# Optimization experiments

Measured on AMD Instinct MI355X. Metric: run time of the kernel, lower is better.

The kernel has to match this reference:

```python
import jax, jax.numpy as jnp
import numpy as np

B, TK, H = 32, 1024, 512
N = 2 * H          # hidden_dim * 2
AD = 512           # attention_dimension


def setup_inputs() -> dict:
    key = jax.random.key(0)
    ks = jax.random.split(key, 11)
    s = 0.02  # weight scale
    return {
        's_t_hat': jax.random.normal(ks[0], (B, N), jnp.float32),
        'encoder_outputs': jax.random.normal(ks[1], (B, TK, N), jnp.float32),
        'encoder_feature': jax.random.normal(ks[2], (B * TK, N), jnp.float32),
        'enc_padding_mask': jax.random.uniform(ks[3], (B, TK), jnp.float32),
        'coverage': jax.random.uniform(ks[4], (B, TK), jnp.float32),
        'r_i': jax.random.normal(ks[5], (B, TK, AD), jnp.float32),
        'W_s_w': jax.random.normal(ks[6], (N, N), jnp.float32) * s,
        'W_s_b': jax.random.normal(ks[7], (N,), jnp.float32) * s,
        'W_c_w': jax.random.normal(ks[8], (N, 1), jnp.float32) * s,
        'v_w': jax.random.normal(ks[9], (1, N), jnp.float32) * s,
        'W_r_w': jax.random.normal(ks[10], (N, AD), jnp.float32) * s,
    }


def reference(s_t_hat, encoder_outputs, encoder_feature, enc_padding_mask,
              coverage, r_i, W_s_w, W_s_b, W_c_w, v_w, W_r_w):
    b, t_k, n = encoder_outputs.shape
    # decoder feature: W_s(s_t_hat), broadcast over time
    dec_fea = s_t_hat @ W_s_w.T + W_s_b                       # [b, n]
    enc_feat = encoder_feature.reshape(b, t_k, n)             # [b, t_k, n]
    # coverage feature: W_c applied to scalar coverage per position
    cov_feat = coverage[..., None] * W_c_w[:, 0]              # [b, t_k, n]
    e = jnp.tanh(enc_feat + dec_fea[:, None, :] + cov_feat)   # [b, t_k, n]
    scores = jnp.einsum('btn,n->bt', e, v_w[0])               # [b, t_k]
    attn_ = jax.nn.softmax(scores, axis=1) * enc_padding_mask
    attn = attn_ / attn_.sum(1, keepdims=True)                # renormalized
    c_t = jnp.einsum('bt,btn->bn', attn, encoder_outputs)     # [b, n]
    coverage_new = coverage + attn                            # [b, t_k]
    # structural (LSA) branch
    Wrri = jnp.einsum('bta,na->btn', r_i, W_r_w)              # [b, t_k, n]
    e_s = jnp.tanh(Wrri + dec_fea[:, None, :])
    s2 = jnp.einsum('btn,n->bt', e_s, v_w[0])
    a_struct = (jax.nn.softmax(s2, axis=1) * enc_padding_mask)[:, None, :]  # [b,1,t_k]
    c_t_struct = jnp.einsum('bt,btn->bn', a_struct[:, 0], encoder_outputs)  # [b, n]
    return (c_t, attn, coverage_new, c_t_struct, a_struct)
```

## Files before the change

kernel.cpp:

```cpp
#include <hip/hip_runtime.h>
#include <hip/hip_bf16.h>

static constexpr int BB   = 32;
static constexpr int TKK  = 1024;
static constexpr int ND   = 1024;
static constexpr int ADIM = 512;

typedef __attribute__((ext_vector_type(8))) short bf16x8;
typedef __attribute__((ext_vector_type(4))) float f32x4;

__device__ __forceinline__ float fast_tanh(float x) {
  x = fminf(fmaxf(x, -15.f), 15.f);
  float e = __expf(2.f * x);
  return __fdividef(e - 1.f, e + 1.f);
}

__device__ __forceinline__ short f2bf(float x) {
  unsigned u = __float_as_uint(x);
  u += 0x7FFF + ((u >> 16) & 1);
  return (short)(u >> 16);
}

__device__ __forceinline__ void gload_lds16(const void* g, void* l) {
  __builtin_amdgcn_global_load_lds(
      (const __attribute__((address_space(1))) unsigned int*)g,
      (__attribute__((address_space(3))) unsigned int*)l, 16, 0, 0);
}

__global__ __launch_bounds__(256) void k_cvt2(const float* __restrict__ r_i,
    const float* __restrict__ Wr, short* __restrict__ rb, short* __restrict__ wb) {
  size_t bid = blockIdx.x;
  const float* src;
  short* dst;
  size_t i;
  if (bid < 8192) { src = r_i; dst = rb; i = bid * 256 + threadIdx.x; }
  else            { src = Wr;  dst = wb; i = (bid - 8192) * 256 + threadIdx.x; }
  float4 a = ((const float4*)src)[2 * i];
  float4 b = ((const float4*)src)[2 * i + 1];
  bf16x8 h;
  h[0] = f2bf(a.x); h[1] = f2bf(a.y); h[2] = f2bf(a.z); h[3] = f2bf(a.w);
  h[4] = f2bf(b.x); h[5] = f2bf(b.y); h[6] = f2bf(b.z); h[7] = f2bf(b.w);
  ((bf16x8*)dst)[i] = h;
}

__global__ __launch_bounds__(256) void k_decfea(const float* __restrict__ s_t_hat,
    const float* __restrict__ Wsw, const float* __restrict__ Wsb,
    float* __restrict__ dec) {
  int b  = blockIdx.x >> 3;
  int n0 = (blockIdx.x & 7) << 7;
  int w = threadIdx.x >> 6, lane = threadIdx.x & 63;
  const float4* s4 = (const float4*)(s_t_hat + (size_t)b * ND);
  float4 sv0 = s4[lane], sv1 = s4[lane + 64], sv2 = s4[lane + 128], sv3 = s4[lane + 192];
  for (int nn = 0; nn < 32; nn++) {
    int n = n0 + w * 32 + nn;
    const float4* w4 = (const float4*)(Wsw + (size_t)n * ND);
    float4 wa = w4[lane], wb = w4[lane + 64], wc = w4[lane + 128], wd = w4[lane + 192];
    float acc = sv0.x*wa.x + sv0.y*wa.y + sv0.z*wa.z + sv0.w*wa.w
              + sv1.x*wb.x + sv1.y*wb.y + sv1.z*wb.z + sv1.w*wb.w
              + sv2.x*wc.x + sv2.y*wc.y + sv2.z*wc.z + sv2.w*wc.w
              + sv3.x*wd.x + sv3.y*wd.y + sv3.z*wd.z + sv3.w*wd.w;
    #pragma unroll
    for (int off = 32; off; off >>= 1) acc += __shfl_down(acc, off);
    if (lane == 0) dec[b * ND + n] = acc + Wsb[n];
  }
}

__global__ __launch_bounds__(256) void k_scoresA(const float* __restrict__ ef,
    const float* __restrict__ dec, const float* __restrict__ Wc,
    const float* __restrict__ vw, const float* __restrict__ cov,
    float* __restrict__ scores) {
  __shared__ float sb[4];
  int bt = blockIdx.x;
  int b  = bt >> 10;
  int tid = threadIdx.x;
  float4 e = *(const float4*)(ef + (size_t)bt * ND + tid * 4);
  float4 d = *(const float4*)(dec + (size_t)b * ND + tid * 4);
  float4 w = *(const float4*)(Wc + tid * 4);
  float4 v = *(const float4*)(vw + tid * 4);
  float c = cov[bt];
  float s = v.x * fast_tanh(e.x + d.x + c * w.x)
          + v.y * fast_tanh(e.y + d.y + c * w.y)
          + v.z * fast_tanh(e.z + d.z + c * w.z)
          + v.w * fast_tanh(e.w + d.w + c * w.w);
  #pragma unroll
  for (int off = 32; off; off >>= 1) s += __shfl_down(s, off);
  if ((tid & 63) == 0) sb[tid >> 6] = s;
  __syncthreads();
  if (tid == 0) scores[bt] = sb[0] + sb[1] + sb[2] + sb[3];
}

__global__ __launch_bounds__(256) void k_softmaxA(const float* __restrict__ scores,
    const float* __restrict__ mask, const float* __restrict__ cov,
    float* __restrict__ attn, float* __restrict__ covnew) {
  __shared__ float sb[4];
  int b = blockIdx.x, tid = threadIdx.x;
  float4 s = *(const float4*)(scores + (size_t)b * TKK + tid * 4);
  float m = fmaxf(fmaxf(s.x, s.y), fmaxf(s.z, s.w));
  #pragma unroll
  for (int off = 32; off; off >>= 1) m = fmaxf(m, __shfl_down(m, off));
  if ((tid & 63) == 0) sb[tid >> 6] = m;
  __syncthreads();
  m = fmaxf(fmaxf(sb[0], sb[1]), fmaxf(sb[2], sb[3]));
  float4 mk = *(const float4*)(mask + (size_t)b * TKK + tid * 4);
  float4 e;
  e.x = __expf(s.x - m) * mk.x;
  e.y = __expf(s.y - m) * mk.y;
  e.z = __expf(s.z - m) * mk.z;
  e.w = __expf(s.w - m) * mk.w;
  float sum = e.x + e.y + e.z + e.w;
  #pragma unroll
  for (int off = 32; off; off >>= 1) sum += __shfl_down(sum, off);
  __syncthreads();
  if ((tid & 63) == 0) sb[tid >> 6] = sum;
  __syncthreads();
  float inv = __fdividef(1.f, sb[0] + sb[1] + sb[2] + sb[3]);
  float4 a = {e.x * inv, e.y * inv, e.z * inv, e.w * inv};
  *(float4*)(attn + (size_t)b * TKK + tid * 4) = a;
  float4 c = *(const float4*)(cov + (size_t)b * TKK + tid * 4);
  float4 cn = {c.x + a.x, c.y + a.y, c.z + a.z, c.w + a.w};
  *(float4*)(covnew + (size_t)b * TKK + tid * 4) = cn;
}

__global__ __launch_bounds__(256) void k_gemmB3(const short* __restrict__ rb,
    const short* __restrict__ wb, const float* __restrict__ dec,
    const float* __restrict__ vw, float* __restrict__ part) {
  __shared__ __align__(16) short As[3][128 * 32];
  __shared__ __align__(16) short Bs[3][128 * 32];
  const int tid = threadIdx.x;
  const int lane = tid & 63, wv = tid >> 6;
  const int wm = wv >> 1, wn = wv & 1;
  const int g = lane >> 4, cl = lane & 15;
  const int bid = blockIdx.x;
  const int swz = (bid & 7) * 256 + (bid >> 3);
  const int mchunk = swz >> 3, nchunk = swz & 7;
  const int b  = mchunk >> 3;
  const int t0 = (mchunk & 7) * 128;
  const int n0 = nchunk * 128;
  const int lrow4 = lane >> 2;
  const int sck   = ((lane & 3) ^ ((lane >> 3) & 3)) * 8;
  const short* Agbase = rb + (size_t)(b * TKK + t0) * ADIM;
  const short* Bgbase = wb + (size_t)n0 * ADIM;
  const int rdsw = (g ^ ((cl >> 1) & 3)) * 8;

  f32x4 acc[4][4];
  #pragma unroll
  for (int m = 0; m < 4; ++m)
    #pragma unroll
    for (int n = 0; n < 4; ++n) acc[m][n] = (f32x4){0.f, 0.f, 0.f, 0.f};

  auto stage = [&](int buf, int kc) {
    const int k0 = kc * 32;
    #pragma unroll
    for (int p = 0; p < 2; ++p) {
      const int rowc = p * 64 + wv * 16;
      const int row  = rowc + lrow4;
      gload_lds16(Agbase + (size_t)row * ADIM + k0 + sck, &As[buf][rowc * 32]);
      gload_lds16(Bgbase + (size_t)row * ADIM + k0 + sck, &Bs[buf][rowc * 32]);
    }
  };

  stage(0, 0);
  stage(1, 1);
  for (int kc = 0; kc < 16; ++kc) {
    if (kc < 14) {
      stage((kc + 2) % 3, kc + 2);
      asm volatile("s_waitcnt vmcnt(8)" ::: "memory");
    } else if (kc == 14) {
      asm volatile("s_waitcnt vmcnt(4)" ::: "memory");
    } else {
      asm volatile("s_waitcnt vmcnt(0)" ::: "memory");
    }
    __builtin_amdgcn_s_barrier();
    const int cur = kc % 3;
    bf16x8 af[4], bfr[4];
    #pragma unroll
    for (int m = 0; m < 4; ++m)
      af[m] = *(const bf16x8*)&As[cur][(wm * 64 + m * 16 + cl) * 32 + rdsw];
    #pragma unroll
    for (int n = 0; n < 4; ++n)
      bfr[n] = *(const bf16x8*)&Bs[cur][(wn * 64 + n * 16 + cl) * 32 + rdsw];
    #pragma unroll
    for (int m = 0; m < 4; ++m)
      #pragma unroll
      for (int n = 0; n < 4; ++n)
        acc[m][n] = __builtin_amdgcn_mfma_f32_16x16x32_bf16(af[m], bfr[n], acc[m][n], 0, 0, 0);
    __builtin_amdgcn_s_barrier();
  }

  float vvv[4], ddd[4];
  #pragma unroll
  for (int n = 0; n < 4; ++n) {
    const int col = n0 + wn * 64 + n * 16 + cl;
    vvv[n] = vw[col];
    ddd[n] = dec[b * ND + col];
  }
  #pragma unroll
  for (int m = 0; m < 4; ++m) {
    #pragma unroll
    for (int r = 0; r < 4; ++r) {
      float s = 0.f;
      #pragma unroll
      for (int n = 0; n < 4; ++n)
        s += vvv[n] * fast_tanh(acc[m][n][r] + ddd[n]);
      #pragma unroll
      for (int off = 1; off < 16; off <<= 1) s += __shfl_xor(s, off);
      if (cl == 0) {
        const int rowg = b * TKK + t0 + wm * 64 + m * 16 + g * 4 + r;
        part[(size_t)rowg * 16 + nchunk * 2 + wn] = s;
      }
    }
  }
}

__global__ __launch_bounds__(256) void k_gemmB(const float* __restrict__ r_i,
    const float* __restrict__ Wr, const float* __restrict__ dec,
    const float* __restrict__ vw, float* __restrict__ part) {
  __shared__ short As[128 * 64];
  __shared__ short Bs[128 * 64];
  const int tid = threadIdx.x;
  const int lane = tid & 63, wv = tid >> 6;
  const int wm = wv >> 1, wn = wv & 1;
  const int g = lane >> 4, cl = lane & 15;
  const int mchunk = blockIdx.x, nchunk = blockIdx.y;
  const int b  = mchunk >> 3;
  const int t0 = (mchunk & 7) * 128;
  const int n0 = nchunk * 128;
  const float* Ag = r_i + (size_t)(b * TKK + t0) * ADIM;
  const float* Bg = Wr + (size_t)n0 * ADIM;
  const int srow = tid >> 3, skk = (tid & 7) * 8;

  f32x4 acc[4][4];
  #pragma unroll
  for (int m = 0; m < 4; ++m)
    #pragma unroll
    for (int n = 0; n < 4; ++n) acc[m][n] = (f32x4){0.f, 0.f, 0.f, 0.f};

  for (int kc = 0; kc < 8; ++kc) {
    const int k0 = kc * 64;
    __syncthreads();
    #pragma unroll
    for (int dit = 0; dit < 4; ++dit) {
      const int row = dit * 32 + srow;
      const float* sa = Ag + (size_t)row * ADIM + k0 + skk;
      float4 a0 = *(const float4*)sa, a1 = *(const float4*)(sa + 4);
      bf16x8 ha;
      ha[0]=f2bf(a0.x); ha[1]=f2bf(a0.y); ha[2]=f2bf(a0.z); ha[3]=f2bf(a0.w);
      ha[4]=f2bf(a1.x); ha[5]=f2bf(a1.y); ha[6]=f2bf(a1.z); ha[7]=f2bf(a1.w);
      *(bf16x8*)&As[row * 64 + skk] = ha;
      const float* sbp = Bg + (size_t)row * ADIM + k0 + skk;
      float4 b0 = *(const float4*)sbp, b1 = *(const float4*)(sbp + 4);
      bf16x8 hb;
      hb[0]=f2bf(b0.x); hb[1]=f2bf(b0.y); hb[2]=f2bf(b0.z); hb[3]=f2bf(b0.w);
      hb[4]=f2bf(b1.x); hb[5]=f2bf(b1.y); hb[6]=f2bf(b1.z); hb[7]=f2bf(b1.w);
      *(bf16x8*)&Bs[row * 64 + skk] = hb;
    }
    __syncthreads();
    #pragma unroll
    for (int kf = 0; kf < 2; ++kf) {
      bf16x8 af[4], bfr[4];
      #pragma unroll
      for (int m = 0; m < 4; ++m)
        af[m] = *(const bf16x8*)&As[(wm * 64 + m * 16 + cl) * 64 + kf * 32 + g * 8];
      #pragma unroll
      for (int n = 0; n < 4; ++n)
        bfr[n] = *(const bf16x8*)&Bs[(wn * 64 + n * 16 + cl) * 64 + kf * 32 + g * 8];
      #pragma unroll
      for (int m = 0; m < 4; ++m)
        #pragma unroll
        for (int n = 0; n < 4; ++n)
          acc[m][n] = __builtin_amdgcn_mfma_f32_16x16x32_bf16(af[m], bfr[n], acc[m][n], 0, 0, 0);
    }
  }
  float vvv[4], ddd[4];
  #pragma unroll
  for (int n = 0; n < 4; ++n) {
    const int col = n0 + wn * 64 + n * 16 + cl;
    vvv[n] = vw[col];
    ddd[n] = dec[b * ND + col];
  }
  #pragma unroll
  for (int m = 0; m < 4; ++m) {
    #pragma unroll
    for (int r = 0; r < 4; ++r) {
      float s = 0.f;
      #pragma unroll
      for (int n = 0; n < 4; ++n)
        s += vvv[n] * fast_tanh(acc[m][n][r] + ddd[n]);
      #pragma unroll
      for (int off = 1; off < 16; off <<= 1) s += __shfl_xor(s, off);
      if (cl == 0) {
        const int rowg = b * TKK + t0 + wm * 64 + m * 16 + g * 4 + r;
        part[(size_t)rowg * 16 + nchunk * 2 + wn] = s;
      }
    }
  }
}

__global__ __launch_bounds__(256) void k_softmaxB(const float* __restrict__ part,
    const float* __restrict__ mask, float* __restrict__ astruct) {
  __shared__ float sb[4];
  int b = blockIdx.x, tid = threadIdx.x;
  float sv[4];
  #pragma unroll
  for (int tt = 0; tt < 4; ++tt) {
    const float4* pp = (const float4*)(part + ((size_t)b * TKK + tid * 4 + tt) * 16);
    float4 q0 = pp[0], q1 = pp[1], q2 = pp[2], q3 = pp[3];
    sv[tt] = q0.x+q0.y+q0.z+q0.w + q1.x+q1.y+q1.z+q1.w
           + q2.x+q2.y+q2.z+q2.w + q3.x+q3.y+q3.z+q3.w;
  }
  float m = fmaxf(fmaxf(sv[0], sv[1]), fmaxf(sv[2], sv[3]));
  #pragma unroll
  for (int off = 32; off; off >>= 1) m = fmaxf(m, __shfl_down(m, off));
  if ((tid & 63) == 0) sb[tid >> 6] = m;
  __syncthreads();
  m = fmaxf(fmaxf(sb[0], sb[1]), fmaxf(sb[2], sb[3]));
  float e0 = __expf(sv[0] - m), e1 = __expf(sv[1] - m);
  float e2 = __expf(sv[2] - m), e3 = __expf(sv[3] - m);
  float sum = e0 + e1 + e2 + e3;
  #pragma unroll
  for (int off = 32; off; off >>= 1) sum += __shfl_down(sum, off);
  __syncthreads();
  if ((tid & 63) == 0) sb[tid >> 6] = sum;
  __syncthreads();
  float inv = __fdividef(1.f, sb[0] + sb[1] + sb[2] + sb[3]);
  float4 mk = *(const float4*)(mask + (size_t)b * TKK + tid * 4);
  float4 a = {e0 * mk.x * inv, e1 * mk.y * inv, e2 * mk.z * inv, e3 * mk.w * inv};
  *(float4*)(astruct + (size_t)b * TKK + tid * 4) = a;
}

__global__ __launch_bounds__(256) void k_ctx(const float* __restrict__ enc,
    const float* __restrict__ attn, const float* __restrict__ astr,
    float* __restrict__ partials) {
  int tc = blockIdx.x, b = blockIdx.y;
  int tid = threadIdx.x, lane = tid & 63;
  float a1v = attn[(size_t)b * TKK + tc * 64 + lane];
  float a2v = astr[(size_t)b * TKK + tc * 64 + lane];
  const float4* e4 = (const float4*)(enc + (size_t)(b * TKK + tc * 64) * ND);
  float4 ac = {0, 0, 0, 0}, as = {0, 0, 0, 0};
  #pragma unroll 4
  for (int m = 0; m < 64; m++) {
    float a1 = __shfl(a1v, m), a2 = __shfl(a2v, m);
    float4 ev = e4[(size_t)m * 256 + tid];
    ac.x += a1 * ev.x; ac.y += a1 * ev.y; ac.z += a1 * ev.z; ac.w += a1 * ev.w;
    as.x += a2 * ev.x; as.y += a2 * ev.y; as.z += a2 * ev.z; as.w += a2 * ev.w;
  }
  float* p = partials + (size_t)(b * 16 + tc) * 2 * ND;
  *(float4*)(p + tid * 4) = ac;
  *(float4*)(p + ND + tid * 4) = as;
}

__global__ __launch_bounds__(256) void k_reduce(const float* __restrict__ partials,
    float* __restrict__ ct, float* __restrict__ cts) {
  int b = blockIdx.x, tid = threadIdx.x;
  float4 sc = {0, 0, 0, 0}, ss = {0, 0, 0, 0};
  for (int tc = 0; tc < 16; tc++) {
    const float* p = partials + (size_t)(b * 16 + tc) * 2 * ND;
    float4 p1 = *(const float4*)(p + tid * 4);
    float4 p2 = *(const float4*)(p + ND + tid * 4);
    sc.x += p1.x; sc.y += p1.y; sc.z += p1.z; sc.w += p1.w;
    ss.x += p2.x; ss.y += p2.y; ss.z += p2.z; ss.w += p2.w;
  }
  *(float4*)(ct + (size_t)b * ND + tid * 4) = sc;
  *(float4*)(cts + (size_t)b * ND + tid * 4) = ss;
}

extern "C" void kernel_launch(void* const* d_in, const int* in_sizes, int n_in,
                              void* d_out, int out_size, void* d_ws, size_t ws_size,
                              hipStream_t stream) {
  const float* s_t_hat = (const float*)d_in[0];
  const float* enc_out  = (const float*)d_in[1];
  const float* enc_feat = (const float*)d_in[2];
  const float* mask     = (const float*)d_in[3];
  const float* cov      = (const float*)d_in[4];
  const float* r_i      = (const float*)d_in[5];
  const float* Wsw      = (const float*)d_in[6];
  const float* Wsb      = (const float*)d_in[7];
  const float* Wc       = (const float*)d_in[8];
  const float* vw       = (const float*)d_in[9];
  const float* Wr       = (const float*)d_in[10];

  float* out    = (float*)d_out;
  float* ct     = out;
  float* attn   = out + 32768;
  float* covnew = out + 65536;
  float* cts    = out + 98304;
  float* astr   = out + 131072;

  float* ws       = (float*)d_ws;
  float* dec      = ws;
  float* scores   = ws + 32768;
  float* s2part   = ws + 65536;
  float* partials = ws + 589824;
  short* rb       = (short*)(ws + 1638400);
  short* wb       = rb + 16777216;
  const size_t NEEDED = 1638400ull * 4 + 16777216ull * 2 + 524288ull * 2;

  k_decfea<<<256, 256, 0, stream>>>(s_t_hat, Wsw, Wsb, dec);
  k_scoresA<<<BB * TKK, 256, 0, stream>>>(enc_feat, dec, Wc, vw, cov, scores);
  k_softmaxA<<<BB, 256, 0, stream>>>(scores, mask, cov, attn, covnew);
  if (ws_size >= NEEDED) {
    k_cvt2<<<8448, 256, 0, stream>>>(r_i, Wr, rb, wb);
    k_gemmB3<<<2048, 256, 0, stream>>>(rb, wb, dec, vw, s2part);
  } else {
    k_gemmB<<<dim3(256, 8), 256, 0, stream>>>(r_i, Wr, dec, vw, s2part);
  }
  k_softmaxB<<<BB, 256, 0, stream>>>(s2part, mask, astr);
  k_ctx<<<dim3(16, BB), 256, 0, stream>>>(enc_out, attn, astr, partials);
  k_reduce<<<BB, 256, 0, stream>>>(partials, ct, cts);
}
```

Before: 172.0 us.

## Load GEMM B fragments from global into registers, wave-per-row scores, coarser ctx blocks

The bf16 GEMM no longer stages the weight tile in LDS. Each wave reads its B fragments straight from global memory into double-buffered registers, so LDS use and shared traffic drop by half, with the vmcnt waits retuned to match. The scores kernel now gives one wave per (b,t) row instead of one block, which removes the shared-memory reduction and its barrier. The context kernel covers 128 timesteps per block, halving the partials that the reduce step must sum. The cost is more global reads of B, which rely on cache reuse, and higher register pressure.

```diff
diff --git a/kernel.cpp b/kernel.cpp
--- a/kernel.cpp
+++ b/kernel.cpp
@@ -69,24 +69,26 @@
     const float* __restrict__ dec, const float* __restrict__ Wc,
     const float* __restrict__ vw, const float* __restrict__ cov,
     float* __restrict__ scores) {
-  __shared__ float sb[4];
-  int bt = blockIdx.x;
-  int b  = bt >> 10;
-  int tid = threadIdx.x;
-  float4 e = *(const float4*)(ef + (size_t)bt * ND + tid * 4);
-  float4 d = *(const float4*)(dec + (size_t)b * ND + tid * 4);
-  float4 w = *(const float4*)(Wc + tid * 4);
-  float4 v = *(const float4*)(vw + tid * 4);
-  float c = cov[bt];
-  float s = v.x * fast_tanh(e.x + d.x + c * w.x)
-          + v.y * fast_tanh(e.y + d.y + c * w.y)
-          + v.z * fast_tanh(e.z + d.z + c * w.z)
-          + v.w * fast_tanh(e.w + d.w + c * w.w);
+  const int bt = blockIdx.x * 4 + (threadIdx.x >> 6);
+  const int b  = bt >> 10;
+  const int lane = threadIdx.x & 63;
+  const float c = cov[bt];
+  float s = 0.f;
+  #pragma unroll
+  for (int q = 0; q < 4; ++q) {
+    const int col = q * 256 + lane * 4;
+    float4 e = *(const float4*)(ef + (size_t)bt * ND + col);
+    float4 d = *(const float4*)(dec + (size_t)b * ND + col);
+    float4 w = *(const float4*)(Wc + col);
+    float4 v = *(const float4*)(vw + col);
+    s += v.x * fast_tanh(e.x + d.x + c * w.x)
+       + v.y * fast_tanh(e.y + d.y + c * w.y)
+       + v.z * fast_tanh(e.z + d.z + c * w.z)
+       + v.w * fast_tanh(e.w + d.w + c * w.w);
+  }
   #pragma unroll
   for (int off = 32; off; off >>= 1) s += __shfl_down(s, off);
-  if ((tid & 63) == 0) sb[tid >> 6] = s;
-  __syncthreads();
-  if (tid == 0) scores[bt] = sb[0] + sb[1] + sb[2] + sb[3];
+  if (lane == 0) scores[bt] = s;
 }
 
 __global__ __launch_bounds__(256) void k_softmaxA(const float* __restrict__ scores,
@@ -121,11 +123,10 @@
   *(float4*)(covnew + (size_t)b * TKK + tid * 4) = cn;
 }
 
-__global__ __launch_bounds__(256) void k_gemmB3(const short* __restrict__ rb,
+__global__ __launch_bounds__(256) void k_gemmB5(const short* __restrict__ rb,
     const short* __restrict__ wb, const float* __restrict__ dec,
     const float* __restrict__ vw, float* __restrict__ part) {
   __shared__ __align__(16) short As[3][128 * 32];
-  __shared__ __align__(16) short Bs[3][128 * 32];
   const int tid = threadIdx.x;
   const int lane = tid & 63, wv = tid >> 6;
   const int wm = wv >> 1, wn = wv & 1;
@@ -139,51 +140,58 @@
   const int lrow4 = lane >> 2;
   const int sck   = ((lane & 3) ^ ((lane >> 3) & 3)) * 8;
   const short* Agbase = rb + (size_t)(b * TKK + t0) * ADIM;
-  const short* Bgbase = wb + (size_t)n0 * ADIM;
   const int rdsw = (g ^ ((cl >> 1) & 3)) * 8;
 
+  const short* Bp[4];
+  #pragma unroll
+  for (int n = 0; n < 4; ++n)
+    Bp[n] = wb + (size_t)(n0 + wn * 64 + n * 16 + cl) * ADIM + g * 8;
+
   f32x4 acc[4][4];
   #pragma unroll
   for (int m = 0; m < 4; ++m)
     #pragma unroll
     for (int n = 0; n < 4; ++n) acc[m][n] = (f32x4){0.f, 0.f, 0.f, 0.f};
 
-  auto stage = [&](int buf, int kc) {
+  auto stageA = [&](int buf, int kc) {
     const int k0 = kc * 32;
     #pragma unroll
     for (int p = 0; p < 2; ++p) {
       const int rowc = p * 64 + wv * 16;
-      const int row  = rowc + lrow4;
-      gload_lds16(Agbase + (size_t)row * ADIM + k0 + sck, &As[buf][rowc * 32]);
-      gload_lds16(Bgbase + (size_t)row * ADIM + k0 + sck, &Bs[buf][rowc * 32]);
+      gload_lds16(Agbase + (size_t)(rowc + lrow4) * ADIM + k0 + sck,
+                  &As[buf][rowc * 32]);
     }
   };
 
-  stage(0, 0);
-  stage(1, 1);
+  bf16x8 bfr[2][4];
+  stageA(0, 0);
+  stageA(1, 1);
+  #pragma unroll
+  for (int n = 0; n < 4; ++n) bfr[0][n] = *(const bf16x8*)(Bp[n]);
+
+  #pragma unroll
   for (int kc = 0; kc < 16; ++kc) {
-    if (kc < 14) {
-      stage((kc + 2) % 3, kc + 2);
-      asm volatile("s_waitcnt vmcnt(8)" ::: "memory");
-    } else if (kc == 14) {
-      asm volatile("s_waitcnt vmcnt(4)" ::: "memory");
-    } else {
-      asm volatile("s_waitcnt vmcnt(0)" ::: "memory");
-    }
+    if (kc < 14) stageA((kc + 2) % 3, kc + 2);
+    if (kc < 15) {
+      #pragma unroll
+      for (int n = 0; n < 4; ++n)
+        bfr[(kc + 1) & 1][n] = *(const bf16x8*)(Bp[n] + (kc + 1) * 32);
+    }
+    if (kc < 14)       asm volatile("s_waitcnt vmcnt(6)" ::: "memory");
+    else if (kc == 14) asm volatile("s_waitcnt vmcnt(4)" ::: "memory");
+    else               asm volatile("s_waitcnt vmcnt(0)" ::: "memory");
     __builtin_amdgcn_s_barrier();
     const int cur = kc % 3;
-    bf16x8 af[4], bfr[4];
+    bf16x8 af[4];
     #pragma unroll
     for (int m = 0; m < 4; ++m)
       af[m] = *(const bf16x8*)&As[cur][(wm * 64 + m * 16 + cl) * 32 + rdsw];
     #pragma unroll
-    for (int n = 0; n < 4; ++n)
-      bfr[n] = *(const bf16x8*)&Bs[cur][(wn * 64 + n * 16 + cl) * 32 + rdsw];
-    #pragma unroll
     for (int m = 0; m < 4; ++m)
       #pragma unroll
       for (int n = 0; n < 4; ++n)
-        acc[m][n] = __builtin_amdgcn_mfma_f32_16x16x32_bf16(af[m], bfr[n], acc[m][n], 0, 0, 0);
+        acc[m][n] = __builtin_amdgcn_mfma_f32_16x16x32_bf16(
+            af[m], bfr[kc & 1][n], acc[m][n], 0, 0, 0);
     __builtin_amdgcn_s_barrier();
   }
 
@@ -333,18 +341,21 @@
     float* __restrict__ partials) {
   int tc = blockIdx.x, b = blockIdx.y;
   int tid = threadIdx.x, lane = tid & 63;
-  float a1v = attn[(size_t)b * TKK + tc * 64 + lane];
-  float a2v = astr[(size_t)b * TKK + tc * 64 + lane];
-  const float4* e4 = (const float4*)(enc + (size_t)(b * TKK + tc * 64) * ND);
+  const float4* e4 = (const float4*)(enc + (size_t)(b * TKK + tc * 128) * ND);
   float4 ac = {0, 0, 0, 0}, as = {0, 0, 0, 0};
-  #pragma unroll 4
-  for (int m = 0; m < 64; m++) {
-    float a1 = __shfl(a1v, m), a2 = __shfl(a2v, m);
-    float4 ev = e4[(size_t)m * 256 + tid];
-    ac.x += a1 * ev.x; ac.y += a1 * ev.y; ac.z += a1 * ev.z; ac.w += a1 * ev.w;
-    as.x += a2 * ev.x; as.y += a2 * ev.y; as.z += a2 * ev.z; as.w += a2 * ev.w;
-  }
-  float* p = partials + (size_t)(b * 16 + tc) * 2 * ND;
+  #pragma unroll
+  for (int h = 0; h < 2; ++h) {
+    float a1v = attn[(size_t)b * TKK + tc * 128 + h * 64 + lane];
+    float a2v = astr[(size_t)b * TKK + tc * 128 + h * 64 + lane];
+    #pragma unroll 4
+    for (int m = 0; m < 64; m++) {
+      float a1 = __shfl(a1v, m), a2 = __shfl(a2v, m);
+      float4 ev = e4[(size_t)(h * 64 + m) * 256 + tid];
+      ac.x += a1 * ev.x; ac.y += a1 * ev.y; ac.z += a1 * ev.z; ac.w += a1 * ev.w;
+      as.x += a2 * ev.x; as.y += a2 * ev.y; as.z += a2 * ev.z; as.w += a2 * ev.w;
+    }
+  }
+  float* p = partials + (size_t)(b * 8 + tc) * 2 * ND;
   *(float4*)(p + tid * 4) = ac;
   *(float4*)(p + ND + tid * 4) = as;
 }
@@ -353,8 +364,8 @@
     float* __restrict__ ct, float* __restrict__ cts) {
   int b = blockIdx.x, tid = threadIdx.x;
   float4 sc = {0, 0, 0, 0}, ss = {0, 0, 0, 0};
-  for (int tc = 0; tc < 16; tc++) {
-    const float* p = partials + (size_t)(b * 16 + tc) * 2 * ND;
+  for (int tc = 0; tc < 8; tc++) {
+    const float* p = partials + (size_t)(b * 8 + tc) * 2 * ND;
     float4 p1 = *(const float4*)(p + tid * 4);
     float4 p2 = *(const float4*)(p + ND + tid * 4);
     sc.x += p1.x; sc.y += p1.y; sc.z += p1.z; sc.w += p1.w;
@@ -396,15 +407,15 @@
   const size_t NEEDED = 1638400ull * 4 + 16777216ull * 2 + 524288ull * 2;
 
   k_decfea<<<256, 256, 0, stream>>>(s_t_hat, Wsw, Wsb, dec);
-  k_scoresA<<<BB * TKK, 256, 0, stream>>>(enc_feat, dec, Wc, vw, cov, scores);
+  k_scoresA<<<8192, 256, 0, stream>>>(enc_feat, dec, Wc, vw, cov, scores);
   k_softmaxA<<<BB, 256, 0, stream>>>(scores, mask, cov, attn, covnew);
   if (ws_size >= NEEDED) {
     k_cvt2<<<8448, 256, 0, stream>>>(r_i, Wr, rb, wb);
-    k_gemmB3<<<2048, 256, 0, stream>>>(rb, wb, dec, vw, s2part);
+    k_gemmB5<<<2048, 256, 0, stream>>>(rb, wb, dec, vw, s2part);
   } else {
     k_gemmB<<<dim3(256, 8), 256, 0, stream>>>(r_i, Wr, dec, vw, s2part);
   }
   k_softmaxB<<<BB, 256, 0, stream>>>(s2part, mask, astr);
-  k_ctx<<<dim3(16, BB), 256, 0, stream>>>(enc_out, attn, astr, partials);
+  k_ctx<<<dim3(8, BB), 256, 0, stream>>>(enc_out, attn, astr, partials);
   k_reduce<<<BB, 256, 0, stream>>>(partials, ct, cts);
 }
```

Result: slower. 192.7 us (+12.1%).
